# Optimization experiments

Measured on AMD Instinct MI355X. Metric: run time of the kernel, lower is better.

Reference implementation:

```python
import jax, jax.numpy as jnp
import numpy as np

VQ_DIM = 4          # vq_dim
S_BIT = 8           # scale quantizer bits
K = 1024            # 2 ** vq_b
FEEDBACK_FEATURE = 64


def setup_inputs() -> dict:
    key = jax.random.key(0)
    k1, k2 = jax.random.split(key)
    feedback = jax.random.normal(k1, (32, 16, 512), dtype=jnp.float32)
    # nn.Parameter(randn(k, d)) then reset_embed(): embed / sqrt(feedback_feature) * 4
    embed = jax.random.normal(k2, (K, VQ_DIM), dtype=jnp.float32) / np.sqrt(FEEDBACK_FEATURE) * 4.0
    return {"feedback": feedback, "embed": embed}


def _float_biter(x):
    # FloatBiter.forward: quantize to S_BIT bits in log4 space, straight-through.
    dot_base = (2.0 ** jnp.arange(S_BIT)).astype(jnp.float32)  # [S_BIT]
    xc = jnp.clip(x + 1.0, 1.0, 16.0)[..., None]
    lg = jnp.log(xc) / np.float32(np.log(4.0))               # in [0, 2]
    bits = jnp.floor(lg * dot_base).astype(jnp.int32) % 2     # torch .long() truncation (x >= 0)
    x1 = jnp.power(4.0, (bits.astype(jnp.float32) / dot_base).sum(-1)) - 1.0
    return x + jax.lax.stop_gradient(x1 - x)


def reference(feedback, embed):
    b, p, D = feedback.shape
    g = D // VQ_DIM
    scale = jnp.linalg.norm(feedback, axis=-1)        # [b, p]
    scale_q = _float_biter(scale)                      # [b, p]
    fn = (feedback / scale[..., None]).reshape(b, p, g, VQ_DIM)
    xx = jnp.sum(fn * fn, axis=-1)                     # [b, p, g]
    ee = jnp.sum(embed * embed, axis=-1)               # [K]
    xe = jnp.einsum('bpgd,kd->bpgk', fn, embed)        # [b, p, g, K]
    dist = (xx[..., None] - 2.0 * xe + ee) / VQ_DIM
    ind = jnp.argmin(dist, axis=-1)                    # [b, p, g]
    fqn = embed[ind]                                   # [b, p, g, VQ_DIM]
    # dist(.,.).mean(-1).mean().mean() == full mean of squared diff
    loss1 = jnp.mean((fqn - jax.lax.stop_gradient(fn)) ** 2)
    loss2 = jnp.mean((jax.lax.stop_gradient(fqn) - fn) ** 2)
    fq = fqn.reshape(b, p, D) * scale_q[..., None]
    out = feedback + jax.lax.stop_gradient(fq - feedback)  # straight-through
    return out, loss1, loss2
```

## Files before the change

### kernel.cpp

```cpp
#include <hip/hip_runtime.h>
#include <math.h>

#define ROWS 512
#define DIMS 512
#define KCODES 1024
#define NGRP 128
#define NT 256

__global__ __launch_bounds__(NT) void vq_main(const float* __restrict__ feedback,
                                              const float* __restrict__ embed,
                                              float* __restrict__ out,
                                              float* __restrict__ partial)
{
    __shared__ float4 s_code[KCODES];
    __shared__ float  s_ee[KCODES];
    __shared__ float  s_f[DIMS];
    __shared__ float  s_dp[NGRP * 16];
    __shared__ int    s_ip[NGRP * 16];
    __shared__ float  s_red[4];

    const int row = blockIdx.x;
    const int tid = threadIdx.x;
    const float* frow = feedback + row * DIMS;

    #pragma unroll
    for (int r = 0; r < 4; ++r) {
        int k = tid + r * NT;
        float4 e = ((const float4*)embed)[k];
        s_code[k] = make_float4(-2.f * e.x, -2.f * e.y, -2.f * e.z, -2.f * e.w);
        s_ee[k] = e.x * e.x + e.y * e.y + e.z * e.z + e.w * e.w;
    }

    float2 f2 = ((const float2*)frow)[tid];
    ((float2*)s_f)[tid] = f2;
    float ss = f2.x * f2.x + f2.y * f2.y;
    #pragma unroll
    for (int off = 32; off > 0; off >>= 1) ss += __shfl_down(ss, off, 64);
    if ((tid & 63) == 0) s_red[tid >> 6] = ss;
    __syncthreads();
    const float sumsq = s_red[0] + s_red[1] + s_red[2] + s_red[3];
    const float scale = sqrtf(sumsq);
    const float inv   = 1.0f / scale;

    float xc = fminf(fmaxf(scale + 1.0f, 1.0f), 16.0f);
    float lg = log2f(xc) * 0.5f;
    float sbits = 0.f, base = 1.f;
    #pragma unroll
    for (int i = 0; i < 8; ++i) {
        int b = ((int)floorf(lg * base)) & 1;
        sbits += (float)b / base;
        base *= 2.f;
    }
    const float scale_q = exp2f(2.0f * sbits) - 1.0f;

    const int j = tid & 15;
    const int c = tid >> 4;
    float fn[32];
    #pragma unroll
    for (int i = 0; i < 8; ++i) {
        float4 v = ((float4*)s_f)[j * 8 + i];
        fn[4 * i + 0] = v.x * inv; fn[4 * i + 1] = v.y * inv;
        fn[4 * i + 2] = v.z * inv; fn[4 * i + 3] = v.w * inv;
    }
    float dmin[8]; int kmin[8];
    #pragma unroll
    for (int jj = 0; jj < 8; ++jj) { dmin[jj] = 1e30f; kmin[jj] = 0; }

    const int kbeg = c * 64;
    for (int k = kbeg; k < kbeg + 64; ++k) {
        float4 cc = s_code[k];
        float  ee = s_ee[k];
        #pragma unroll
        for (int jj = 0; jj < 8; ++jj) {
            float d = fmaf(cc.x, fn[4 * jj + 0],
                      fmaf(cc.y, fn[4 * jj + 1],
                      fmaf(cc.z, fn[4 * jj + 2],
                      fmaf(cc.w, fn[4 * jj + 3], ee))));
            if (d < dmin[jj]) { dmin[jj] = d; kmin[jj] = k; }
        }
    }

    #pragma unroll
    for (int jj = 0; jj < 8; ++jj) {
        int g = j * 8 + jj;
        s_dp[g * 16 + c] = dmin[jj];
        s_ip[g * 16 + c] = kmin[jj];
    }
    __syncthreads();

    float lsum = 0.f;
    if (tid < NGRP) {
        const int g = tid;
        float dm = s_dp[g * 16 + 0];
        int   km = s_ip[g * 16 + 0];
        #pragma unroll
        for (int cc2 = 1; cc2 < 16; ++cc2) {
            float dv = s_dp[g * 16 + cc2];
            int   kv = s_ip[g * 16 + cc2];
            if (dv < dm) { dm = dv; km = kv; }
        }
        float4 code = s_code[km];
        float e0 = -0.5f * code.x, e1 = -0.5f * code.y,
              e2 = -0.5f * code.z, e3 = -0.5f * code.w;
        float4 fv = ((float4*)s_f)[g];
        float x0 = fv.x * inv, x1 = fv.y * inv, x2 = fv.z * inv, x3 = fv.w * inv;
        float d0 = e0 - x0, d1 = e1 - x1, d2 = e2 - x2, d3 = e3 - x3;
        lsum = d0 * d0 + d1 * d1 + d2 * d2 + d3 * d3;
        ((float4*)out)[row * NGRP + g] =
            make_float4(e0 * scale_q, e1 * scale_q, e2 * scale_q, e3 * scale_q);
    }
    #pragma unroll
    for (int off = 32; off > 0; off >>= 1) lsum += __shfl_down(lsum, off, 64);
    __syncthreads();
    if ((tid & 63) == 0 && tid < NGRP) s_red[tid >> 6] = lsum;
    __syncthreads();
    if (tid == 0) partial[row] = s_red[0] + s_red[1];
}

__global__ __launch_bounds__(256) void vq_finish(const float* __restrict__ partial,
                                                 float* __restrict__ out_loss)
{
    __shared__ float r[4];
    float v = partial[threadIdx.x] + partial[threadIdx.x + 256];
    #pragma unroll
    for (int off = 32; off > 0; off >>= 1) v += __shfl_down(v, off, 64);
    if ((threadIdx.x & 63) == 0) r[threadIdx.x >> 6] = v;
    __syncthreads();
    if (threadIdx.x == 0) {
        float t = (r[0] + r[1] + r[2] + r[3]) / 262144.f;
        out_loss[0] = t;
        out_loss[1] = t;
    }
}

extern "C" void kernel_launch(void* const* d_in, const int* in_sizes, int n_in,
                              void* d_out, int out_size, void* d_ws, size_t ws_size,
                              hipStream_t stream) {
    const float* feedback = (const float*)d_in[0];
    const float* embed    = (const float*)d_in[1];
    float* out     = (float*)d_out;
    float* partial = (float*)d_ws;

    vq_main<<<ROWS, NT, 0, stream>>>(feedback, embed, out, partial);
    vq_finish<<<1, 256, 0, stream>>>(partial, out + ROWS * DIMS);
}
```

Measured before the change: 72.54 us.

## Pack distance and index into integer key, use packed FMA and padded LDS

After: 69.59 us. 4.1% less time.

```diff
diff --git a/kernel.cpp b/kernel.cpp
--- a/kernel.cpp
+++ b/kernel.cpp
@@ -7,31 +7,32 @@
 #define NGRP 128
 #define NT 256
 
+typedef float v2f __attribute__((ext_vector_type(2)));
+
 __global__ __launch_bounds__(NT) void vq_main(const float* __restrict__ feedback,
                                               const float* __restrict__ embed,
                                               float* __restrict__ out,
                                               float* __restrict__ partial)
 {
-    __shared__ float4 s_code[KCODES];
-    __shared__ float  s_ee[KCODES];
+    __shared__ float4 s_code[KCODES + 16];
+    __shared__ float  s_ee[KCODES + 16];
     __shared__ float  s_f[DIMS];
-    __shared__ float  s_dp[NGRP * 16];
-    __shared__ int    s_ip[NGRP * 16];
+    __shared__ int    s_kp[NGRP * 16];
     __shared__ float  s_red[4];
 
     const int row = blockIdx.x;
     const int tid = threadIdx.x;
-    const float* frow = feedback + row * DIMS;
 
     #pragma unroll
     for (int r = 0; r < 4; ++r) {
         int k = tid + r * NT;
+        int kp = k + (k >> 6);
         float4 e = ((const float4*)embed)[k];
-        s_code[k] = make_float4(-2.f * e.x, -2.f * e.y, -2.f * e.z, -2.f * e.w);
-        s_ee[k] = e.x * e.x + e.y * e.y + e.z * e.z + e.w * e.w;
+        s_code[kp] = make_float4(-2.f * e.x, -2.f * e.y, -2.f * e.z, -2.f * e.w);
+        s_ee[kp] = e.x * e.x + e.y * e.y + e.z * e.z + e.w * e.w + 4.0f;
     }
 
-    float2 f2 = ((const float2*)frow)[tid];
+    float2 f2 = ((const float2*)(feedback + row * DIMS))[tid];
     ((float2*)s_f)[tid] = f2;
     float ss = f2.x * f2.x + f2.y * f2.y;
     #pragma unroll
@@ -55,58 +56,59 @@
 
     const int j = tid & 15;
     const int c = tid >> 4;
-    float fn[32];
+    v2f fnp[4][4];
     #pragma unroll
-    for (int i = 0; i < 8; ++i) {
-        float4 v = ((float4*)s_f)[j * 8 + i];
-        fn[4 * i + 0] = v.x * inv; fn[4 * i + 1] = v.y * inv;
-        fn[4 * i + 2] = v.z * inv; fn[4 * i + 3] = v.w * inv;
+    for (int p = 0; p < 4; ++p) {
+        float4 a = ((float4*)s_f)[j * 8 + 2 * p];
+        float4 b = ((float4*)s_f)[j * 8 + 2 * p + 1];
+        fnp[p][0] = (v2f){a.x * inv, b.x * inv};
+        fnp[p][1] = (v2f){a.y * inv, b.y * inv};
+        fnp[p][2] = (v2f){a.z * inv, b.z * inv};
+        fnp[p][3] = (v2f){a.w * inv, b.w * inv};
     }
-    float dmin[8]; int kmin[8];
+    int keymin[8];
     #pragma unroll
-    for (int jj = 0; jj < 8; ++jj) { dmin[jj] = 1e30f; kmin[jj] = 0; }
+    for (int i = 0; i < 8; ++i) keymin[i] = 0x7FFFFFFF;
 
-    const int kbeg = c * 64;
-    for (int k = kbeg; k < kbeg + 64; ++k) {
-        float4 cc = s_code[k];
-        float  ee = s_ee[k];
+    const float4* codeP = s_code + c * 65;
+    const float*  eeP   = s_ee   + c * 65;
+    const int kbase = c * 64;
+    #pragma unroll 4
+    for (int i = 0; i < 64; ++i) {
+        float4 cc = codeP[i];
+        float  eb = eeP[i];
+        int kk = kbase + i;
         #pragma unroll
-        for (int jj = 0; jj < 8; ++jj) {
-            float d = fmaf(cc.x, fn[4 * jj + 0],
-                      fmaf(cc.y, fn[4 * jj + 1],
-                      fmaf(cc.z, fn[4 * jj + 2],
-                      fmaf(cc.w, fn[4 * jj + 3], ee))));
-            if (d < dmin[jj]) { dmin[jj] = d; kmin[jj] = k; }
+        for (int p = 0; p < 4; ++p) {
+            v2f acc = (v2f){eb, eb};
+            acc = __builtin_elementwise_fma((v2f){cc.x, cc.x}, fnp[p][0], acc);
+            acc = __builtin_elementwise_fma((v2f){cc.y, cc.y}, fnp[p][1], acc);
+            acc = __builtin_elementwise_fma((v2f){cc.z, cc.z}, fnp[p][2], acc);
+            acc = __builtin_elementwise_fma((v2f){cc.w, cc.w}, fnp[p][3], acc);
+            int k0 = (__float_as_int(acc.x) & 0xFFFFFC00) | kk;
+            int k1 = (__float_as_int(acc.y) & 0xFFFFFC00) | kk;
+            keymin[2 * p]     = min(keymin[2 * p],     k0);
+            keymin[2 * p + 1] = min(keymin[2 * p + 1], k1);
         }
     }
-
     #pragma unroll
-    for (int jj = 0; jj < 8; ++jj) {
-        int g = j * 8 + jj;
-        s_dp[g * 16 + c] = dmin[jj];
-        s_ip[g * 16 + c] = kmin[jj];
-    }
+    for (int p = 0; p < 8; ++p) s_kp[(j * 8 + p) * 16 + c] = keymin[p];
     __syncthreads();
 
     float lsum = 0.f;
     if (tid < NGRP) {
-        const int g = tid;
-        float dm = s_dp[g * 16 + 0];
-        int   km = s_ip[g * 16 + 0];
+        int key = s_kp[tid * 16];
         #pragma unroll
-        for (int cc2 = 1; cc2 < 16; ++cc2) {
-            float dv = s_dp[g * 16 + cc2];
-            int   kv = s_ip[g * 16 + cc2];
-            if (dv < dm) { dm = dv; km = kv; }
-        }
-        float4 code = s_code[km];
+        for (int c2 = 1; c2 < 16; ++c2) key = min(key, s_kp[tid * 16 + c2]);
+        int km = key & 1023;
+        float4 code = s_code[km + (km >> 6)];
         float e0 = -0.5f * code.x, e1 = -0.5f * code.y,
               e2 = -0.5f * code.z, e3 = -0.5f * code.w;
-        float4 fv = ((float4*)s_f)[g];
+        float4 fv = ((float4*)s_f)[tid];
         float x0 = fv.x * inv, x1 = fv.y * inv, x2 = fv.z * inv, x3 = fv.w * inv;
         float d0 = e0 - x0, d1 = e1 - x1, d2 = e2 - x2, d3 = e3 - x3;
         lsum = d0 * d0 + d1 * d1 + d2 * d2 + d3 * d3;
-        ((float4*)out)[row * NGRP + g] =
+        ((float4*)out)[row * NGRP + tid] =
             make_float4(e0 * scale_q, e1 * scale_q, e2 * scale_q, e3 * scale_q);
     }
     #pragma unroll
```
